# Performance work log

Hardware: AMD Instinct MI355X
Metric: run time of the kernel (lower is better)

The kernel has to match this reference:

```python
import jax, jax.numpy as jnp
import numpy as np

NUM_CLASSES = 512  # P distinct identities in the batch (labels are in [0, P))
TAU = 0.5
EPS = 1e-12


def _l2norm(x):
    # F.normalize(x, dim=1) with eps clamp
    n = jnp.sqrt(jnp.sum(x * x, axis=1, keepdims=True))
    return x / jnp.maximum(n, EPS)


def setup_inputs() -> dict:
    key = jax.random.key(0)
    k1, k2, k3 = jax.random.split(key, 3)
    N, D, P = 8192, 2048, NUM_CLASSES
    feat_vp = jax.random.normal(k1, (N, D), dtype=jnp.float32)
    feat_ap = jax.random.normal(k2, (N, D), dtype=jnp.float32)
    feat_rp = jax.random.normal(k3, (N, D), dtype=jnp.float32)
    # P identities, K = N/P instances each; every class present
    label = (jnp.arange(N) % P).astype(jnp.int32)
    return {"feat_vp": feat_vp, "feat_ap": feat_ap, "feat_rp": feat_rp, "label": label}


def reference(feat_vp, feat_ap, feat_rp, label):
    P = NUM_CLASSES
    fv = _l2norm(feat_vp)
    fa = _l2norm(feat_ap)
    fr = _l2norm(feat_rp)

    # segment-mean over labels (replaces the O(N^2 D) python loop)
    counts = jax.ops.segment_sum(jnp.ones_like(label, dtype=fv.dtype), label,
                                 num_segments=P)  # [P]
    inv_cnt = 1.0 / counts[:, None]

    def centers(f):
        s = jax.ops.segment_sum(f, label, num_segments=P)  # [P, D]
        return _l2norm(s * inv_cnt)

    cv, ca, cr = centers(fv), centers(fa), centers(fr)

    # per-sample centers = unique centers gathered back by label
    loss_intra = (jnp.sum((fv - cv[label]) ** 2, axis=1).mean()
                  + jnp.sum((fa - ca[label]) ** 2, axis=1).mean()
                  + jnp.sum((fr - cr[label]) ** 2, axis=1).mean())

    def pair_loss(c1, c2):
        logits = (c1 @ c2.T) / TAU  # [P, P]
        logp = jax.nn.log_softmax(logits, axis=1)
        return -jnp.mean(jnp.diagonal(logp))

    loss_inter = pair_loss(cv, ca) + pair_loss(cv, cr) + pair_loss(ca, cr)
    return loss_intra + loss_inter
```

## Files before the change

kernel.cpp:

```cpp
#include <hip/hip_runtime.h>
#include <hip/hip_bf16.h>

#define P_CLS 512
#define D_DIM 2048
#define CAP   32
#define TAU_INV 2.0f

typedef short short8 __attribute__((ext_vector_type(8)));
typedef float f32x4 __attribute__((ext_vector_type(4)));

__device__ __forceinline__ unsigned short f2bf_bits(float x) {
  __hip_bfloat16 b = __float2bfloat16(x);
  unsigned short u;
  __builtin_memcpy(&u, &b, sizeof(u));
  return u;
}

__device__ __forceinline__ float xred_sum(float v) {
#pragma unroll
  for (int o = 1; o < 64; o <<= 1) v += __shfl_xor(v, o, 64);
  return v;
}
__device__ __forceinline__ float xred_max(float v) {
#pragma unroll
  for (int o = 1; o < 64; o <<= 1) v = fmaxf(v, __shfl_xor(v, o, 64));
  return v;
}

__global__ __launch_bounds__(1024)
void k_prep(const int* __restrict__ label, int* __restrict__ cnt,
            int* __restrict__ idx, float* __restrict__ accs, int n) {
  __shared__ int lcnt[P_CLS];
  int t = threadIdx.x;
  if (t < P_CLS) lcnt[t] = 0;
  if (t >= P_CLS && t < P_CLS + 8) accs[t - P_CLS] = 0.f;
  __syncthreads();
  for (int i = t; i < n; i += 1024) {
    int p = label[i];
    int slot = atomicAdd(&lcnt[p], 1);
    if (slot < CAP) idx[p * CAP + slot] = i;
  }
  __syncthreads();
  if (t < P_CLS) cnt[t] = lcnt[t];
}

__global__ __launch_bounds__(256, 4)
void k_centers(const float* __restrict__ f0, const float* __restrict__ f1,
               const float* __restrict__ f2, const int* __restrict__ cnt,
               const int* __restrict__ idx, __hip_bfloat16* __restrict__ cb,
               float* __restrict__ accs) {
  __shared__ f32x4 scr[2][4][2];
  __shared__ float s2s[4];
  int p = blockIdx.x, m = blockIdx.y;
  const float* F = (m == 0) ? f0 : (m == 1) ? f1 : f2;
  int t = threadIdx.x, lane = t & 63, wv = t >> 6;
  int c = cnt[p];
  if (c > CAP) c = CAP;
  const int* idxp = idx + p * CAP;
  int col0 = wv * 512 + lane * 4;
  f32x4 acc0 = {0, 0, 0, 0}, acc1 = {0, 0, 0, 0};
  int ng = (c + 7) >> 3;
  for (int g = 0; g < ng; ++g) {
    int rbase = g * 8;
    f32x4 v0[8], v1[8];
#pragma unroll
    for (int j = 0; j < 8; ++j) {
      int rr = rbase + j;
      if (rr >= c) rr = c - 1;
      const float* rp = F + (long)idxp[rr] * D_DIM + col0;
      v0[j] = *(const f32x4*)rp;
      v1[j] = *(const f32x4*)(rp + 256);
    }
    f32x4 sa, sb;
#pragma unroll
    for (int j = 0; j < 4; ++j) {
      f32x4 qa = v0[j] * v0[j] + v1[j] * v1[j];
      sa[j] = qa.x + qa.y + qa.z + qa.w;
      f32x4 qb = v0[j + 4] * v0[j + 4] + v1[j + 4] * v1[j + 4];
      sb[j] = qb.x + qb.y + qb.z + qb.w;
    }
#pragma unroll
    for (int o = 1; o < 64; o <<= 1) {
#pragma unroll
      for (int j = 0; j < 4; ++j) {
        sa[j] += __shfl_xor(sa[j], o, 64);
        sb[j] += __shfl_xor(sb[j], o, 64);
      }
    }
    int par = g & 1;
    if (lane == 0) {
      scr[par][wv][0] = sa;
      scr[par][wv][1] = sb;
    }
    __syncthreads();
    f32x4 ta = scr[par][0][0] + scr[par][1][0] + scr[par][2][0] + scr[par][3][0];
    f32x4 tb = scr[par][0][1] + scr[par][1][1] + scr[par][2][1] + scr[par][3][1];
#pragma unroll
    for (int j = 0; j < 8; ++j) {
      float tot = (j < 4) ? ta[j] : tb[j - 4];
      float w = (rbase + j < c) ? (1.0f / fmaxf(sqrtf(tot), 1e-12f)) : 0.f;
      acc0 += v0[j] * w;
      acc1 += v1[j] * w;
    }
  }
  f32x4 q = acc0 * acc0 + acc1 * acc1;
  float s2 = q.x + q.y + q.z + q.w;
  s2 = xred_sum(s2);
  if (lane == 0) s2s[wv] = s2;
  __syncthreads();
  float sn = sqrtf(s2s[0] + s2s[1] + s2s[2] + s2s[3]);
  float inv = 1.0f / fmaxf(sn, 1e-12f);
  __hip_bfloat16* dst = cb + ((long)m * P_CLS + p) * D_DIM;
  f32x4 o0 = acc0 * inv, o1 = acc1 * inv;
  ushort4 h0, h1;
  h0.x = f2bf_bits(o0.x); h0.y = f2bf_bits(o0.y);
  h0.z = f2bf_bits(o0.z); h0.w = f2bf_bits(o0.w);
  h1.x = f2bf_bits(o1.x); h1.y = f2bf_bits(o1.y);
  h1.z = f2bf_bits(o1.z); h1.w = f2bf_bits(o1.w);
  *(ushort4*)(dst + col0) = h0;
  *(ushort4*)(dst + col0 + 256) = h1;
  if (t == 0 && c > 0) atomicAdd(&accs[0], sn);
}

__global__ __launch_bounds__(256)
void k_gemm(const __hip_bfloat16* __restrict__ cbh, float* __restrict__ logits) {
  __shared__ __align__(16) unsigned short As[2][64 * 40], Bs[2][64 * 40];
  int pair = blockIdx.y, kz = blockIdx.z, nkz = gridDim.z;
  int ksl = D_DIM / nkz;
  int ma = (pair == 2) ? 1 : 0;
  int mb = (pair == 0) ? 1 : 2;
  const unsigned short* A =
      (const unsigned short*)cbh + (long)ma * P_CLS * D_DIM + kz * ksl;
  const unsigned short* B =
      (const unsigned short*)cbh + (long)mb * P_CLS * D_DIM + kz * ksl;
  float* C = logits + ((long)kz * 3 + pair) * P_CLS * P_CLS;
  int tm = (blockIdx.x >> 3) * 64, tn = (blockIdx.x & 7) * 64;
  int t = threadIdx.x, lane = t & 63, wv = t >> 6;
  int srow = t >> 2, skc = (t & 3) * 8;
  int quad = lane >> 4, mr = lane & 15;
  const unsigned short* pa = A + (long)(tm + srow) * D_DIM + skc;
  const unsigned short* pb = B + (long)(tn + srow) * D_DIM + skc;
  f32x4 acc[4] = {{0,0,0,0},{0,0,0,0},{0,0,0,0},{0,0,0,0}};
  uint4 av = *(const uint4*)pa, bv = *(const uint4*)pb;
  *(uint4*)(&As[0][srow * 40 + skc]) = av;
  *(uint4*)(&Bs[0][srow * 40 + skc]) = bv;
  av = *(const uint4*)(pa + 32); bv = *(const uint4*)(pb + 32);
  const int NIT = ksl / 32;
  for (int it = 0; it < NIT; ++it) {
    __syncthreads();
    int cur = it & 1;
    if (it + 1 < NIT) {
      *(uint4*)(&As[cur ^ 1][srow * 40 + skc]) = av;
      *(uint4*)(&Bs[cur ^ 1][srow * 40 + skc]) = bv;
    }
    if (it + 2 < NIT) {
      av = *(const uint4*)(pa + (it + 2) * 32);
      bv = *(const uint4*)(pb + (it + 2) * 32);
    }
    short8 af = *(const short8*)(&As[cur][(wv * 16 + mr) * 40 + quad * 8]);
#pragma unroll
    for (int nb = 0; nb < 4; ++nb) {
      short8 bfr = *(const short8*)(&Bs[cur][(nb * 16 + mr) * 40 + quad * 8]);
      acc[nb] = __builtin_amdgcn_mfma_f32_16x16x32_bf16(af, bfr, acc[nb], 0, 0, 0);
    }
  }
  int crow = tm + wv * 16 + quad * 4;
#pragma unroll
  for (int nb = 0; nb < 4; ++nb)
#pragma unroll
    for (int r = 0; r < 4; ++r)
      C[(long)(crow + r) * P_CLS + tn + nb * 16 + mr] = acc[nb][r] * TAU_INV;
}

__global__ __launch_bounds__(256)
void k_lse(const float* __restrict__ logits, float* __restrict__ accs, int nkz) {
  __shared__ float sred[8];
  int row = blockIdx.x;
  int p = row & (P_CLS - 1);
  int t = threadIdx.x, lane = t & 63, wv = t >> 6;
  float v0 = 0.f, v1 = 0.f;
  for (int z = 0; z < nkz; ++z) {
    const float* L = logits + ((long)z * 3 * P_CLS + row) * P_CLS;
    v0 += L[t];
    v1 += L[t + 256];
  }
  float mx = xred_max(fmaxf(v0, v1));
  if (lane == 0) sred[wv] = mx;
  __syncthreads();
  mx = fmaxf(fmaxf(sred[0], sred[1]), fmaxf(sred[2], sred[3]));
  float e = expf(v0 - mx) + expf(v1 - mx);
  e = xred_sum(e);
  if (lane == 0) sred[4 + wv] = e;
  __syncthreads();
  if (t == 0) {
    float tot = sred[4] + sred[5] + sred[6] + sred[7];
    float diag = 0.f;
    for (int z = 0; z < nkz; ++z)
      diag += logits[((long)z * 3 * P_CLS + row) * P_CLS + p];
    atomicAdd(&accs[1], mx + logf(tot) - diag);
  }
}

__global__ void k_final(const float* __restrict__ accs, float* __restrict__ out,
                        float invN) {
  out[0] = 6.0f - 2.0f * invN * accs[0] + accs[1] * (1.0f / (float)P_CLS);
}

extern "C" void kernel_launch(void* const* d_in, const int* in_sizes, int n_in,
                              void* d_out, int out_size, void* d_ws, size_t ws_size,
                              hipStream_t stream) {
  const float* fvp = (const float*)d_in[0];
  const float* fap = (const float*)d_in[1];
  const float* frp = (const float*)d_in[2];
  const int* label = (const int*)d_in[3];
  int N = in_sizes[3];

  char* ws = (char*)d_ws;
  int* cnt = (int*)ws;
  int* idx = (int*)(ws + 2048);
  float* accs = (float*)(ws + 2048 + 65536);
  __hip_bfloat16* cb = (__hip_bfloat16*)(ws + 131072);
  float* logits = (float*)(ws + 131072 + 3ul * P_CLS * D_DIM * 2);

  size_t base = 131072 + 3ul * P_CLS * D_DIM * 2;
  size_t per_z = 3ul * P_CLS * P_CLS * 4;
  int KZ = (ws_size >= base + 4 * per_z) ? 4 : 2;

  hipLaunchKernelGGL(k_prep, dim3(1), dim3(1024), 0, stream, label, cnt, idx,
                     accs, N);
  hipLaunchKernelGGL(k_centers, dim3(P_CLS, 3), dim3(256), 0, stream,
                     fvp, fap, frp, cnt, idx, cb, accs);
  hipLaunchKernelGGL(k_gemm, dim3(64, 3, KZ), dim3(256), 0, stream, cb, logits);
  hipLaunchKernelGGL(k_lse, dim3(3 * P_CLS), dim3(256), 0, stream, logits, accs, KZ);
  hipLaunchKernelGGL(k_final, dim3(1), dim3(1), 0, stream, accs, (float*)d_out,
                     1.0f / (float)N);
}
```

Baseline: 249.8 us.

## Fuse label bucketing into centers kernel and replace atomics with final reduction

Result: faster. 240.1 us (-3.9%).

```diff
diff --git a/kernel.cpp b/kernel.cpp
--- a/kernel.cpp
+++ b/kernel.cpp
@@ -27,50 +27,79 @@
   return v;
 }
 
-__global__ __launch_bounds__(1024)
-void k_prep(const int* __restrict__ label, int* __restrict__ cnt,
-            int* __restrict__ idx, float* __restrict__ accs, int n) {
-  __shared__ int lcnt[P_CLS];
-  int t = threadIdx.x;
-  if (t < P_CLS) lcnt[t] = 0;
-  if (t >= P_CLS && t < P_CLS + 8) accs[t - P_CLS] = 0.f;
-  __syncthreads();
-  for (int i = t; i < n; i += 1024) {
-    int p = label[i];
-    int slot = atomicAdd(&lcnt[p], 1);
-    if (slot < CAP) idx[p * CAP + slot] = i;
-  }
-  __syncthreads();
-  if (t < P_CLS) cnt[t] = lcnt[t];
-}
-
 __global__ __launch_bounds__(256, 4)
 void k_centers(const float* __restrict__ f0, const float* __restrict__ f1,
-               const float* __restrict__ f2, const int* __restrict__ cnt,
-               const int* __restrict__ idx, __hip_bfloat16* __restrict__ cb,
-               float* __restrict__ accs) {
+               const float* __restrict__ f2, const int* __restrict__ label,
+               int n, __hip_bfloat16* __restrict__ cb,
+               float* __restrict__ snorm) {
+  __shared__ int lidx[CAP];
+  __shared__ int lcnt;
   __shared__ f32x4 scr[2][4][2];
   __shared__ float s2s[4];
   int p = blockIdx.x, m = blockIdx.y;
   const float* F = (m == 0) ? f0 : (m == 1) ? f1 : f2;
   int t = threadIdx.x, lane = t & 63, wv = t >> 6;
-  int c = cnt[p];
+  if (t == 0) lcnt = 0;
+  __syncthreads();
+  for (int j = t; j < n; j += 256) {
+    if (label[j] == p) {
+      int s_ = atomicAdd(&lcnt, 1);
+      if (s_ < CAP) lidx[s_] = j;
+    }
+  }
+  __syncthreads();
+  int c = lcnt;
   if (c > CAP) c = CAP;
-  const int* idxp = idx + p * CAP;
-  int col0 = wv * 512 + lane * 4;
+
+  unsigned voff = (unsigned)((wv * 512 + lane * 4) * 4);
   f32x4 acc0 = {0, 0, 0, 0}, acc1 = {0, 0, 0, 0};
   int ng = (c + 7) >> 3;
   for (int g = 0; g < ng; ++g) {
     int rbase = g * 8;
+    const float* b0;
+    const float* b1;
+    const float* b2;
+    const float* b3;
+    const float* b4;
+    const float* b5;
+    const float* b6;
+    const float* b7;
+#define ROWPTR(J, B)                                        \
+    {                                                       \
+      int rr = rbase + J;                                   \
+      if (rr >= c) rr = c - 1;                              \
+      int ri = __builtin_amdgcn_readfirstlane(lidx[rr]);    \
+      B = F + (long)ri * D_DIM;                             \
+    }
+    ROWPTR(0, b0) ROWPTR(1, b1) ROWPTR(2, b2) ROWPTR(3, b3)
+    ROWPTR(4, b4) ROWPTR(5, b5) ROWPTR(6, b6) ROWPTR(7, b7)
+#undef ROWPTR
     f32x4 v0[8], v1[8];
-#pragma unroll
-    for (int j = 0; j < 8; ++j) {
-      int rr = rbase + j;
-      if (rr >= c) rr = c - 1;
-      const float* rp = F + (long)idxp[rr] * D_DIM + col0;
-      v0[j] = *(const f32x4*)rp;
-      v1[j] = *(const f32x4*)(rp + 256);
-    }
+    asm volatile(
+        "global_load_dwordx4 %0, %24, %16\n\t"
+        "global_load_dwordx4 %8, %24, %16 offset:1024\n\t"
+        "global_load_dwordx4 %1, %24, %17\n\t"
+        "global_load_dwordx4 %9, %24, %17 offset:1024\n\t"
+        "global_load_dwordx4 %2, %24, %18\n\t"
+        "global_load_dwordx4 %10, %24, %18 offset:1024\n\t"
+        "global_load_dwordx4 %3, %24, %19\n\t"
+        "global_load_dwordx4 %11, %24, %19 offset:1024\n\t"
+        "global_load_dwordx4 %4, %24, %20\n\t"
+        "global_load_dwordx4 %12, %24, %20 offset:1024\n\t"
+        "global_load_dwordx4 %5, %24, %21\n\t"
+        "global_load_dwordx4 %13, %24, %21 offset:1024\n\t"
+        "global_load_dwordx4 %6, %24, %22\n\t"
+        "global_load_dwordx4 %14, %24, %22 offset:1024\n\t"
+        "global_load_dwordx4 %7, %24, %23\n\t"
+        "global_load_dwordx4 %15, %24, %23 offset:1024\n\t"
+        "s_waitcnt vmcnt(0)"
+        : "=v"(v0[0]), "=v"(v0[1]), "=v"(v0[2]), "=v"(v0[3]),
+          "=v"(v0[4]), "=v"(v0[5]), "=v"(v0[6]), "=v"(v0[7]),
+          "=v"(v1[0]), "=v"(v1[1]), "=v"(v1[2]), "=v"(v1[3]),
+          "=v"(v1[4]), "=v"(v1[5]), "=v"(v1[6]), "=v"(v1[7])
+        : "s"(b0), "s"(b1), "s"(b2), "s"(b3),
+          "s"(b4), "s"(b5), "s"(b6), "s"(b7), "v"(voff)
+        : "memory");
     f32x4 sa, sb;
 #pragma unroll
     for (int j = 0; j < 4; ++j) {
@@ -110,6 +139,7 @@
   __syncthreads();
   float sn = sqrtf(s2s[0] + s2s[1] + s2s[2] + s2s[3]);
   float inv = 1.0f / fmaxf(sn, 1e-12f);
+  int col0 = wv * 512 + lane * 4;
   __hip_bfloat16* dst = cb + ((long)m * P_CLS + p) * D_DIM;
   f32x4 o0 = acc0 * inv, o1 = acc1 * inv;
   ushort4 h0, h1;
@@ -119,7 +149,7 @@
   h1.z = f2bf_bits(o1.z); h1.w = f2bf_bits(o1.w);
   *(ushort4*)(dst + col0) = h0;
   *(ushort4*)(dst + col0 + 256) = h1;
-  if (t == 0 && c > 0) atomicAdd(&accs[0], sn);
+  if (t == 0) snorm[m * P_CLS + p] = (c > 0) ? sn : 0.f;
 }
 
 __global__ __launch_bounds__(256)
@@ -173,7 +203,8 @@
 }
 
 __global__ __launch_bounds__(256)
-void k_lse(const float* __restrict__ logits, float* __restrict__ accs, int nkz) {
+void k_lse(const float* __restrict__ logits, float* __restrict__ rowloss,
+           int nkz) {
   __shared__ float sred[8];
   int row = blockIdx.x;
   int p = row & (P_CLS - 1);
@@ -197,13 +228,29 @@
     float diag = 0.f;
     for (int z = 0; z < nkz; ++z)
       diag += logits[((long)z * 3 * P_CLS + row) * P_CLS + p];
-    atomicAdd(&accs[1], mx + logf(tot) - diag);
-  }
-}
-
-__global__ void k_final(const float* __restrict__ accs, float* __restrict__ out,
-                        float invN) {
-  out[0] = 6.0f - 2.0f * invN * accs[0] + accs[1] * (1.0f / (float)P_CLS);
+    rowloss[row] = mx + logf(tot) - diag;
+  }
+}
+
+__global__ __launch_bounds__(256)
+void k_final(const float* __restrict__ snorm, const float* __restrict__ rowloss,
+             float* __restrict__ out, float invN) {
+  __shared__ float sh[8];
+  int t = threadIdx.x, lane = t & 63, wv = t >> 6;
+  float s = 0.f, l = 0.f;
+  for (int j = t; j < 3 * P_CLS; j += 256) {
+    s += snorm[j];
+    l += rowloss[j];
+  }
+  s = xred_sum(s);
+  l = xred_sum(l);
+  if (lane == 0) { sh[wv] = s; sh[4 + wv] = l; }
+  __syncthreads();
+  if (t == 0) {
+    float st = sh[0] + sh[1] + sh[2] + sh[3];
+    float lt = sh[4] + sh[5] + sh[6] + sh[7];
+    out[0] = 6.0f - 2.0f * invN * st + lt * (1.0f / (float)P_CLS);
+  }
 }
 
 extern "C" void kernel_launch(void* const* d_in, const int* in_sizes, int n_in,
@@ -216,22 +263,20 @@
   int N = in_sizes[3];
 
   char* ws = (char*)d_ws;
-  int* cnt = (int*)ws;
-  int* idx = (int*)(ws + 2048);
-  float* accs = (float*)(ws + 2048 + 65536);
-  __hip_bfloat16* cb = (__hip_bfloat16*)(ws + 131072);
-  float* logits = (float*)(ws + 131072 + 3ul * P_CLS * D_DIM * 2);
-
-  size_t base = 131072 + 3ul * P_CLS * D_DIM * 2;
+  float* snorm = (float*)ws;
+  float* rowloss = (float*)(ws + 8192);
+  __hip_bfloat16* cb = (__hip_bfloat16*)(ws + 16384);
+  float* logits = (float*)(ws + 16384 + 3ul * P_CLS * D_DIM * 2);
+
+  size_t base = 16384 + 3ul * P_CLS * D_DIM * 2;
   size_t per_z = 3ul * P_CLS * P_CLS * 4;
   int KZ = (ws_size >= base + 4 * per_z) ? 4 : 2;
 
-  hipLaunchKernelGGL(k_prep, dim3(1), dim3(1024), 0, stream, label, cnt, idx,
-                     accs, N);
   hipLaunchKernelGGL(k_centers, dim3(P_CLS, 3), dim3(256), 0, stream,
-                     fvp, fap, frp, cnt, idx, cb, accs);
+                     fvp, fap, frp, label, N, cb, snorm);
   hipLaunchKernelGGL(k_gemm, dim3(64, 3, KZ), dim3(256), 0, stream, cb, logits);
-  hipLaunchKernelGGL(k_lse, dim3(3 * P_CLS), dim3(256), 0, stream, logits, accs, KZ);
-  hipLaunchKernelGGL(k_final, dim3(1), dim3(1), 0, stream, accs, (float*)d_out,
-                     1.0f / (float)N);
-}
+  hipLaunchKernelGGL(k_lse, dim3(3 * P_CLS), dim3(256), 0, stream, logits,
+                     rowloss, KZ);
+  hipLaunchKernelGGL(k_final, dim3(1), dim3(256), 0, stream, snorm, rowloss,
+                     (float*)d_out, 1.0f / (float)N);
+}
```
